# Kernel tuning notes

Measured on AMD Instinct MI355X. Metric: run time of the kernel, lower is better.

## Reference

```python
import jax, jax.numpy as jnp
import numpy as np

T, D, R, C, L = 4096, 512, 32, 32, 2  # time, input, trace, context, num_blocks
NEG_SLOPE = 0.01
EPS = 1e-5  # eqx LayerNorm default


def _layernorm(x, g, b):
    m = jnp.mean(x, -1, keepdims=True)
    v = jnp.var(x, -1, keepdims=True)
    return g * (x - m) * jax.lax.rsqrt(v + EPS) + b


def _ffa_scan(a, b, pre, s0, start):
    # a:[R], b:[C], pre:[T,R,C] real>=0, s0:[1,R,C] complex64, start:[T] bool
    ab = jax.lax.complex(jnp.broadcast_to(-jnp.abs(a)[:, None], (R, C)),
                         jnp.broadcast_to(b[None, :], (R, C)))  # log decay+rotation
    ts = jnp.concatenate([jnp.zeros((1,), jnp.float32), jnp.ones((T,), jnp.float32)])
    vals = jnp.concatenate([s0, pre.astype(jnp.complex64)], axis=0)  # [T+1,R,C]
    rst = jnp.concatenate([jnp.zeros((1,), bool), start])

    def op(l, r):
        tl, sl, dl = l
        tr, sr, dr = r
        decay = jnp.exp(ab[None, :, :] * tr[:, None, None])  # gamma^{t_r}
        s = jnp.where(dr[:, None, None], sr, sr + sl * decay)
        t = jnp.where(dr, tr, tl + tr)
        return (t, s, dl | dr)

    _, states, _ = jax.lax.associative_scan(op, (ts, vals, rst))
    return states[1:]  # [T,R,C]


def _forward(x, start_b, state_real, state_imag, Wt, Wc, a, b,
             W0, b0, g0, beta0, W1, b1, g1, beta1):
    h = x
    z = x
    for i in range(L):
        tr = h @ Wt[i].T  # [T,R]
        ct = h @ Wc[i].T  # [T,R] (source maps context proj to trace_size too; R==C)
        pre = jnp.abs(tr[:, :, None] * ct[:, None, :])  # [T,R,C] outer product
        pre = pre / (1e-8 + jnp.sum(pre, axis=(-2, -1), keepdims=True))
        s0 = jax.lax.complex(state_real[i], state_imag[i])  # [1,R,C]
        states = _ffa_scan(a[i], b[i], pre, s0, start_b)
        s = states.reshape(T, R * C)
        mag = jnp.log1p(jnp.abs(s))
        ang = jnp.angle(s)
        scaled = jnp.concatenate([mag * jnp.sin(ang), mag * jnp.cos(ang)], axis=-1)  # [T,2RC]
        z = jax.nn.leaky_relu(_layernorm(scaled @ W0[i].T + b0[i], g0[i], beta0[i]), NEG_SLOPE)
        z = jax.nn.leaky_relu(_layernorm(z @ W1[i].T + b1[i], g1[i], beta1[i]), NEG_SLOPE)
        h = h + z  # residual feeds next block; NSFFM returns last block's z
    return z


def setup_inputs() -> dict:
    key = jax.random.key(0)
    ks = jax.random.split(key, 8)
    x = jax.random.normal(ks[0], (T, D), jnp.float32)
    start = jax.random.randint(ks[1], (T,), 0, 2).astype(jnp.int32)
    next_done = jax.random.randint(ks[2], (T,), 0, 2).astype(jnp.int32)
    Wt = jax.random.normal(ks[3], (L, R, D), jnp.float32) / np.sqrt(D)
    Wc = jax.random.normal(ks[4], (L, R, D), jnp.float32) / np.sqrt(D)
    # ffa.init: a = linspace decays, b = log-spaced angular frequencies
    a = jnp.broadcast_to(jnp.linspace(1e-6, 0.5, R, dtype=jnp.float32)[None], (L, R)).copy()
    b = jnp.broadcast_to((2 * jnp.pi / jnp.exp(jnp.linspace(np.log(1.0), np.log(1024.0), C))).astype(jnp.float32)[None], (L, C)).copy()
    W0 = jax.random.normal(ks[5], (L, D, 2 * R * C), jnp.float32) * 0.01  # default_init scale=0.01
    W1 = jax.random.normal(ks[6], (L, D, D), jnp.float32) / np.sqrt(D)
    return {
        'x': x, 'start': start, 'next_done': next_done,
        'state_real': jnp.zeros((L, 1, R, C), jnp.float32),
        'state_imag': jnp.zeros((L, 1, R, C), jnp.float32),
        'Wt': Wt, 'Wc': Wc, 'a': a, 'b': b,
        'W0': W0, 'b0': jnp.zeros((L, D), jnp.float32),
        'g0': jnp.ones((L, D), jnp.float32), 'beta0': jnp.zeros((L, D), jnp.float32),
        'W1': W1, 'b1': jnp.zeros((L, D), jnp.float32),
        'g1': jnp.ones((L, D), jnp.float32), 'beta1': jnp.zeros((L, D), jnp.float32),
    }


def reference(x, start, next_done, state_real, state_imag, Wt, Wc, a, b,
              W0, b0, g0, beta0, W1, b1, g1, beta1):
    del next_done  # not used in the scan math (kept for interface parity)
    start_b = start.astype(bool)
    return _forward(x, start_b, state_real, state_imag, Wt, Wc, a, b,
                    W0, b0, g0, beta0, W1, b1, g1, beta1)
```

## Files before the change

kernel.cpp:

```cpp
#include <hip/hip_runtime.h>
#include <math.h>

#define TT 4096
#define DD 512
#define RR 32
#define CC 32
#define RC 1024
#define LL 2
#define CHUNK 32
#define NCHUNK 128
#define NEG_SLOPE 0.01f
#define LN_EPS 1e-5f

typedef __attribute__((ext_vector_type(8))) __bf16 bf16x8;
typedef __attribute__((ext_vector_type(4))) float f32x4;

__device__ __forceinline__ unsigned short f2bf(float f) {
    unsigned int u = __builtin_bit_cast(unsigned int, f);
    u += 0x7fffu + ((u >> 16) & 1u);
    return (unsigned short)(u >> 16);
}

__device__ __forceinline__ void gload16(const unsigned short* g, unsigned short* l) {
    __builtin_amdgcn_global_load_lds(
        (const __attribute__((address_space(1))) unsigned int*)(const void*)g,
        (__attribute__((address_space(3))) unsigned int*)(void*)l,
        16, 0, 0);
}

#define NX4  524288
#define NW04 524288
#define NW14 131072
#define NCV  (NX4 + NW04 + NW14)
#define NPK  16384
__global__ __launch_bounds__(256) void setup_kernel(const float4* __restrict__ x,
                                                    const float4* __restrict__ W0,
                                                    const float4* __restrict__ W1,
                                                    const float* __restrict__ Wt,
                                                    const float* __restrict__ Wc,
                                                    ushort4* __restrict__ xb,
                                                    ushort4* __restrict__ W0b,
                                                    ushort4* __restrict__ W1b,
                                                    ushort4* __restrict__ Wtc) {
    int i = blockIdx.x * 256 + threadIdx.x;
    float4 v;
    ushort4* dst;
    int j;
    if (i < NCV) {
        const float4* src;
        if (i < NX4) { src = x; dst = xb; j = i; }
        else if (i < NX4 + NW04) { src = W0; dst = W0b; j = i - NX4; }
        else { src = W1; dst = W1b; j = i - NX4 - NW04; }
        v = src[j];
    } else {
        int ii = i - NCV;
        if (ii >= NPK) return;
        int e = ii * 4;
        int l = e >> 15;
        int r = (e >> 9) & 63;
        int k = e & 511;
        v = (r < 32) ? *(const float4*)&Wt[((size_t)l * 32 + r) * 512 + k]
                     : *(const float4*)&Wc[((size_t)l * 32 + (r - 32)) * 512 + k];
        dst = Wtc; j = ii;
    }
    ushort4 o;
    o.x = f2bf(v.x); o.y = f2bf(v.y); o.z = f2bf(v.z); o.w = f2bf(v.w);
    dst[j] = o;
}

__global__ __launch_bounds__(256) void proj_denom_kernel(const unsigned short* __restrict__ A,
                                                         const unsigned short* __restrict__ B,
                                                         float* __restrict__ tcabs) {
    __shared__ __align__(16) unsigned short As[64 * 32];
    __shared__ __align__(16) unsigned short Bs[64 * 32];
    const int tid = threadIdx.x;
    const int w = tid >> 6, lane = tid & 63;
    const int bm = blockIdx.x * 64;
    const int K = 512;
    const int srow = tid >> 2;
    const int sl = tid & 3;
    const int sswz = (sl ^ ((srow >> 1) & 3)) * 8;
    const unsigned short* gA = A + (size_t)(bm + srow) * K + sl * 8;
    const unsigned short* gB = B + (size_t)srow * K + sl * 8;
    const int wA = srow * 32 + sswz;
    const int wB = srow * 32 + sswz;
    const int fr = lane & 15, hi = lane >> 4;
    const int kslot = hi ^ ((fr >> 1) & 3);
    f32x4 acc0 = {}, acc1 = {}, acc2 = {}, acc3 = {};

    uint4 va = *(const uint4*)gA;
    uint4 vb = *(const uint4*)gB;
    for (int k0 = 0; k0 < K; k0 += 32) {
        __syncthreads();
        *(uint4*)&As[wA] = va;
        *(uint4*)&Bs[wB] = vb;
        __syncthreads();
        if (k0 + 32 < K) {
            va = *(const uint4*)(gA + k0 + 32);
            vb = *(const uint4*)(gB + k0 + 32);
        }
        const int arow = w * 16 + fr;
        bf16x8 af = *(const bf16x8*)&As[arow * 32 + kslot * 8];
        bf16x8 b0 = *(const bf16x8*)&Bs[(0 * 16 + fr) * 32 + kslot * 8];
        bf16x8 b1 = *(const bf16x8*)&Bs[(1 * 16 + fr) * 32 + kslot * 8];
        bf16x8 b2 = *(const bf16x8*)&Bs[(2 * 16 + fr) * 32 + kslot * 8];
        bf16x8 b3 = *(const bf16x8*)&Bs[(3 * 16 + fr) * 32 + kslot * 8];
        acc0 = __builtin_amdgcn_mfma_f32_16x16x32_bf16(af, b0, acc0, 0, 0, 0);
        acc1 = __builtin_amdgcn_mfma_f32_16x16x32_bf16(af, b1, acc1, 0, 0, 0);
        acc2 = __builtin_amdgcn_mfma_f32_16x16x32_bf16(af, b2, acc2, 0, 0, 0);
        acc3 = __builtin_amdgcn_mfma_f32_16x16x32_bf16(af, b3, acc3, 0, 0, 0);
    }
#pragma unroll
    for (int q = 0; q < 4; ++q) {
        float a0 = fabsf(acc0[q]), a1 = fabsf(acc1[q]);
        float a2 = fabsf(acc2[q]), a3 = fabsf(acc3[q]);
        float st = a0 + a1, sc = a2 + a3;
        st += __shfl_xor(st, 1); sc += __shfl_xor(sc, 1);
        st += __shfl_xor(st, 2); sc += __shfl_xor(sc, 2);
        st += __shfl_xor(st, 4); sc += __shfl_xor(sc, 4);
        st += __shfl_xor(st, 8); sc += __shfl_xor(sc, 8);
        float inv = 1.f / (1e-8f + st * sc);
        size_t rb = (size_t)(bm + w * 16 + hi * 4 + q) * 64;
        tcabs[rb + fr]      = a0 * inv;
        tcabs[rb + fr + 16] = a1 * inv;
        tcabs[rb + fr + 32] = a2;
        tcabs[rb + fr + 48] = a3;
    }
}

__global__ __launch_bounds__(256) void scan_pass1(const float* __restrict__ tcabs,
                                                  const int* __restrict__ start,
                                                  const float* __restrict__ a,
                                                  const float* __restrict__ b,
                                                  float4* __restrict__ ab4) {
    int tid = blockIdx.x * 256 + threadIdx.x;
    int rc = tid & (RC - 1);
    int chunk = tid >> 10;
    int r = rc >> 5, c = rc & 31;
    float e = expf(-fabsf(a[r]));
    float gr = e * cosf(b[c]);
    float gi = e * sinf(b[c]);
    float alr = 1.f, ali = 0.f, ber = 0.f, bei = 0.f;
    int t0 = chunk * CHUNK;
    for (int j = 0; j < CHUNK; ++j) {
        int t = t0 + j;
        float pre = tcabs[t * 64 + r] * tcabs[t * 64 + 32 + c];
        if (start[t]) {
            alr = 0.f; ali = 0.f; ber = pre; bei = 0.f;
        } else {
            float nbr = pre + gr * ber - gi * bei;
            float nbi =       gr * bei + gi * ber;
            float nar = gr * alr - gi * ali;
            float nai = gr * ali + gi * alr;
            ber = nbr; bei = nbi; alr = nar; ali = nai;
        }
    }
    ab4[chunk * RC + rc] = make_float4(alr, ali, ber, bei);
}

__global__ __launch_bounds__(256) void scan_pass2f(const float* __restrict__ tcabs,
                                                   const float4* __restrict__ ab4,
                                                   const int* __restrict__ start,
                                                   const float* __restrict__ a,
                                                   const float* __restrict__ b,
                                                   const float* __restrict__ s0r,
                                                   const float* __restrict__ s0i,
                                                   unsigned short* __restrict__ scaled) {
    int bx = blockIdx.x;
    int chunk = bx >> 2;
    int rc = (bx & 3) * 256 + threadIdx.x;
    int r = rc >> 5, c = rc & 31;
    float e = expf(-fabsf(a[r]));
    float gr = e * cosf(b[c]);
    float gi = e * sinf(b[c]);
    float sr = s0r[rc], si = s0i[rc];
    int j = 0;
    for (; j + 8 <= chunk; j += 8) {
        float4 buf[8];
#pragma unroll
        for (int u = 0; u < 8; ++u) buf[u] = ab4[(j + u) * RC + rc];
#pragma unroll
        for (int u = 0; u < 8; ++u) {
            float nsr = buf[u].z + buf[u].x * sr - buf[u].y * si;
            float nsi = buf[u].w + buf[u].x * si + buf[u].y * sr;
            sr = nsr; si = nsi;
        }
    }
    for (; j < chunk; ++j) {
        float4 ab = ab4[j * RC + rc];
        float nsr = ab.z + ab.x * sr - ab.y * si;
        float nsi = ab.w + ab.x * si + ab.y * sr;
        sr = nsr; si = nsi;
    }
    int t0 = chunk * CHUNK;
    for (int jj = 0; jj < CHUNK; ++jj) {
        int t = t0 + jj;
        float pre = tcabs[t * 64 + r] * tcabs[t * 64 + 32 + c];
        if (start[t]) {
            sr = pre; si = 0.f;
        } else {
            float nsr = pre + gr * sr - gi * si;
            float nsi =       gr * si + gi * sr;
            sr = nsr; si = nsi;
        }
        float m = sqrtf(sr * sr + si * si);
        float mag = log1pf(m);
        float f = (m > 0.f) ? (mag / m) : 0.f;
        scaled[(size_t)t * 2048 + rc]        = f2bf(si * f);
        scaled[(size_t)t * 2048 + 1024 + rc] = f2bf(sr * f);
    }
}

template <int K, int N, int SPLITK>
__global__ __launch_bounds__(256) void gemm_bt_mfma(const unsigned short* __restrict__ A,
                                                    const unsigned short* __restrict__ B,
                                                    float* __restrict__ Cm) {
    __shared__ __align__(16) unsigned short As[128 * 32];
    __shared__ __align__(16) unsigned short Bs[64 * 32];
    const int tid = threadIdx.x;
    const int w = tid >> 6, lane = tid & 63;
    const int nwg = gridDim.x * gridDim.y * gridDim.z;
    const int id = blockIdx.x + gridDim.x * (blockIdx.y + gridDim.y * blockIdx.z);
    const int lid = (id & 7) * (nwg >> 3) + (id >> 3);
    const int bxs = lid % gridDim.x;
    const int t2 = lid / gridDim.x;
    const int bys = t2 % gridDim.y;
    const int bzs = t2 / gridDim.y;
    const int bm = bys * 128, bn = bxs * 64;
    const int kbeg = bzs * (K / SPLITK);
    const int kend = kbeg + (K / SPLITK);
    const int wr = w >> 1, wc = w & 1;
    const int lrow = lane >> 2;
    const int sphys = lane & 3;
    const int slog = sphys ^ ((lrow >> 1) & 3);
    const unsigned short* gA0 = A + (size_t)(bm + w * 32 + lrow) * K + slog * 8;
    const unsigned short* gA1 = A + (size_t)(bm + w * 32 + 16 + lrow) * K + slog * 8;
    const unsigned short* gB  = B + (size_t)(bn + w * 16 + lrow) * K + slog * 8;
    unsigned short* lA0 = &As[(w * 32) * 32];
    unsigned short* lA1 = &As[(w * 32 + 16) * 32];
    unsigned short* lB  = &Bs[(w * 16) * 32];
    const int fr = lane & 15, hi = lane >> 4;
    const int kslot = hi ^ ((fr >> 1) & 3);
    f32x4 acc[4][2] = {};

    for (int k0 = kbeg; k0 < kend; k0 += 32) {
        __syncthreads();
        gload16(gA0 + k0, lA0);
        gload16(gA1 + k0, lA1);
        gload16(gB  + k0, lB);
        __syncthreads();
        bf16x8 af[4], bfv[2];
#pragma unroll
        for (int mi = 0; mi < 4; ++mi) {
            int row = wr * 64 + mi * 16 + fr;
            af[mi] = *(const bf16x8*)&As[row * 32 + kslot * 8];
        }
#pragma unroll
        for (int ni = 0; ni < 2; ++ni) {
            int row = wc * 32 + ni * 16 + fr;
            bfv[ni] = *(const bf16x8*)&Bs[row * 32 + kslot * 8];
        }
#pragma unroll
        for (int mi = 0; mi < 4; ++mi)
#pragma unroll
            for (int ni = 0; ni < 2; ++ni)
                acc[mi][ni] = __builtin_amdgcn_mfma_f32_16x16x32_bf16(
                    af[mi], bfv[ni], acc[mi][ni], 0, 0, 0);
    }
    float* Cz = Cm + (size_t)bzs * TT * N;
    const int ccol0 = bn + wc * 32 + fr;
    const int crow0 = bm + wr * 64 + hi * 4;
#pragma unroll
    for (int ni = 0; ni < 2; ++ni) {
        int col = ccol0 + ni * 16;
#pragma unroll
        for (int mi = 0; mi < 4; ++mi)
#pragma unroll
            for (int q = 0; q < 4; ++q)
                Cz[(size_t)(crow0 + mi * 16 + q) * N + col] = acc[mi][ni][q];
    }
}

__global__ __launch_bounds__(256) void ln_lrelu_kernel(const float* __restrict__ y0,
                                                       const float* __restrict__ y1,
                                                       const float* __restrict__ badd,
                                                       const float* __restrict__ g,
                                                       const float* __restrict__ be,
                                                       unsigned short* __restrict__ zb,
                                                       const float* __restrict__ res,
                                                       unsigned short* __restrict__ hbf,
                                                       float* __restrict__ fout) {
    int t = blockIdx.x;
    int tid = threadIdx.x;
    size_t base = (size_t)t * 512;
    float v0 = y0[base + tid] + y1[base + tid] + badd[tid];
    float v1 = y0[base + 256 + tid] + y1[base + 256 + tid] + badd[256 + tid];
    float s = v0 + v1, ss = v0 * v0 + v1 * v1;
#pragma unroll
    for (int o = 32; o > 0; o >>= 1) {
        s  += __shfl_down(s, o);
        ss += __shfl_down(ss, o);
    }
    __shared__ float sh[8];
    __shared__ float mrs[2];
    int wid = tid >> 6, lane = tid & 63;
    if (lane == 0) { sh[wid] = s; sh[4 + wid] = ss; }
    __syncthreads();
    if (tid == 0) {
        float S = sh[0] + sh[1] + sh[2] + sh[3];
        float SS = sh[4] + sh[5] + sh[6] + sh[7];
        float m = S * (1.f / 512.f);
        float var = SS * (1.f / 512.f) - m * m;
        mrs[0] = m;
        mrs[1] = rsqrtf(var + LN_EPS);
    }
    __syncthreads();
    float m = mrs[0], rs = mrs[1];
    float z0 = g[tid] * (v0 - m) * rs + be[tid];
    float z1 = g[256 + tid] * (v1 - m) * rs + be[256 + tid];
    z0 = (z0 > 0.f) ? z0 : NEG_SLOPE * z0;
    z1 = (z1 > 0.f) ? z1 : NEG_SLOPE * z1;
    if (zb)   { zb[base + tid] = f2bf(z0); zb[base + 256 + tid] = f2bf(z1); }
    if (hbf) {
        float h0 = (res ? res[base + tid] : 0.f) + z0;
        float h1 = (res ? res[base + 256 + tid] : 0.f) + z1;
        hbf[base + tid] = f2bf(h0);
        hbf[base + 256 + tid] = f2bf(h1);
    }
    if (fout) { fout[base + tid] = z0; fout[base + 256 + tid] = z1; }
}

extern "C" void kernel_launch(void* const* d_in, const int* in_sizes, int n_in,
                              void* d_out, int out_size, void* d_ws, size_t ws_size,
                              hipStream_t stream) {
    const float* x     = (const float*)d_in[0];
    const int*   start = (const int*)d_in[1];
    const float* s0r = (const float*)d_in[3];
    const float* s0i = (const float*)d_in[4];
    const float* Wt  = (const float*)d_in[5];
    const float* Wc  = (const float*)d_in[6];
    const float* a   = (const float*)d_in[7];
    const float* b   = (const float*)d_in[8];
    const float* W0  = (const float*)d_in[9];
    const float* b0  = (const float*)d_in[10];
    const float* g0  = (const float*)d_in[11];
    const float* be0 = (const float*)d_in[12];
    const float* W1  = (const float*)d_in[13];
    const float* b1  = (const float*)d_in[14];
    const float* g1  = (const float*)d_in[15];
    const float* be1 = (const float*)d_in[16];
    float* out = (float*)d_out;
    float* ws  = (float*)d_ws;

    float* p = ws;
    float* tcabs  = p; p += 262144;
    float4* ab4   = (float4*)p; p += 524288;
    unsigned short* scaled = (unsigned short*)p; p += 4194304;
    float* ybufp  = p; p += 4194304;
    unsigned short* zbuf_bf = (unsigned short*)p; p += 1048576;
    unsigned short* x_bf    = (unsigned short*)p; p += 1048576;
    unsigned short* h_bf    = (unsigned short*)p; p += 1048576;
    unsigned short* Wtcbf   = (unsigned short*)p; p += 32768;
    unsigned short* W0bf    = (unsigned short*)p; p += 1048576;
    unsigned short* W1bf    = (unsigned short*)p; p += 262144;

    setup_kernel<<<(NCV + NPK + 255) / 256, 256, 0, stream>>>(
        (const float4*)x, (const float4*)W0, (const float4*)W1, Wt, Wc,
        (ushort4*)x_bf, (ushort4*)W0bf, (ushort4*)W1bf, (ushort4*)Wtcbf);

    for (int i = 0; i < LL; ++i) {
        const unsigned short* hb = (i == 0) ? x_bf : h_bf;
        proj_denom_kernel<<<64, 256, 0, stream>>>(
            hb, Wtcbf + (size_t)i * 64 * 512, tcabs);
        scan_pass1<<<NCHUNK * RC / 256, 256, 0, stream>>>(
            tcabs, start, a + i * RR, b + i * CC, ab4);
        scan_pass2f<<<NCHUNK * 4, 256, 0, stream>>>(
            tcabs, ab4, start, a + i * RR, b + i * CC,
            s0r + i * RC, s0i + i * RC, scaled);
        gemm_bt_mfma<2048, 512, 2><<<dim3(8, 32, 2), 256, 0, stream>>>(
            scaled, W0bf + (size_t)i * 512 * 2048, ybufp);
        ln_lrelu_kernel<<<TT, 256, 0, stream>>>(
            ybufp, ybufp + (size_t)TT * 512, b0 + i * DD, g0 + i * DD, be0 + i * DD,
            zbuf_bf, nullptr, nullptr, nullptr);
        gemm_bt_mfma<512, 512, 2><<<dim3(8, 32, 2), 256, 0, stream>>>(
            zbuf_bf, W1bf + (size_t)i * 512 * 512, ybufp);
        ln_lrelu_kernel<<<TT, 256, 0, stream>>>(
            ybufp, ybufp + (size_t)TT * 512, b1 + i * DD, g1 + i * DD, be1 + i * DD,
            nullptr,
            (i < LL - 1) ? x : nullptr,
            (i < LL - 1) ? h_bf : nullptr,
            (i == LL - 1) ? out : nullptr);
    }
}
```

Before: 205.6 us.

## Fuse GEMM with LayerNorm epilogue using full-row tiles and double-buffered loads

```diff
diff --git a/kernel.cpp b/kernel.cpp
--- a/kernel.cpp
+++ b/kernel.cpp
@@ -211,123 +211,99 @@
     }
 }
 
-template <int K, int N, int SPLITK>
-__global__ __launch_bounds__(256) void gemm_bt_mfma(const unsigned short* __restrict__ A,
-                                                    const unsigned short* __restrict__ B,
-                                                    float* __restrict__ Cm) {
-    __shared__ __align__(16) unsigned short As[128 * 32];
-    __shared__ __align__(16) unsigned short Bs[64 * 32];
+template <int K>
+__global__ __launch_bounds__(256) void gemm_ln(const unsigned short* __restrict__ A,
+                                               const unsigned short* __restrict__ B,
+                                               const float* __restrict__ bias,
+                                               const float* __restrict__ g,
+                                               const float* __restrict__ be,
+                                               unsigned short* __restrict__ zb,
+                                               const float* __restrict__ res,
+                                               unsigned short* __restrict__ hbf,
+                                               float* __restrict__ fout) {
+    __shared__ __align__(16) unsigned short As[2][16 * 32];
+    __shared__ __align__(16) unsigned short Bs[2][512 * 32];
+    __shared__ float smem_s[16][4];
+    __shared__ float smem_ss[16][4];
     const int tid = threadIdx.x;
     const int w = tid >> 6, lane = tid & 63;
-    const int nwg = gridDim.x * gridDim.y * gridDim.z;
-    const int id = blockIdx.x + gridDim.x * (blockIdx.y + gridDim.y * blockIdx.z);
-    const int lid = (id & 7) * (nwg >> 3) + (id >> 3);
-    const int bxs = lid % gridDim.x;
-    const int t2 = lid / gridDim.x;
-    const int bys = t2 % gridDim.y;
-    const int bzs = t2 / gridDim.y;
-    const int bm = bys * 128, bn = bxs * 64;
-    const int kbeg = bzs * (K / SPLITK);
-    const int kend = kbeg + (K / SPLITK);
-    const int wr = w >> 1, wc = w & 1;
-    const int lrow = lane >> 2;
-    const int sphys = lane & 3;
-    const int slog = sphys ^ ((lrow >> 1) & 3);
-    const unsigned short* gA0 = A + (size_t)(bm + w * 32 + lrow) * K + slog * 8;
-    const unsigned short* gA1 = A + (size_t)(bm + w * 32 + 16 + lrow) * K + slog * 8;
-    const unsigned short* gB  = B + (size_t)(bn + w * 16 + lrow) * K + slog * 8;
-    unsigned short* lA0 = &As[(w * 32) * 32];
-    unsigned short* lA1 = &As[(w * 32 + 16) * 32];
-    unsigned short* lB  = &Bs[(w * 16) * 32];
+    const int bm = blockIdx.x * 16;
     const int fr = lane & 15, hi = lane >> 4;
     const int kslot = hi ^ ((fr >> 1) & 3);
-    f32x4 acc[4][2] = {};
-
-    for (int k0 = kbeg; k0 < kend; k0 += 32) {
+    const int srow = lane >> 2;
+    const int slog = (lane & 3) ^ ((srow >> 1) & 3);
+    const unsigned short* gBb = B + (size_t)(w * 16 + srow) * K + slog * 8;
+    const unsigned short* gAb = A + (size_t)(bm + srow) * K + slog * 8;
+
+    f32x4 acc[8] = {};
+    constexpr int NT = K / 32;
+
+#pragma unroll
+    for (int u = 0; u < 8; ++u)
+        gload16(gBb + (size_t)u * 64 * K, &Bs[0][(size_t)w * 512 + u * 2048]);
+    if (w == 0) gload16(gAb, &As[0][0]);
+    __syncthreads();
+    int cur = 0;
+    for (int t = 0; t < NT; ++t) {
+        if (t + 1 < NT) {
+            const int k0n = (t + 1) * 32;
+            unsigned short* bd = &Bs[cur ^ 1][(size_t)w * 512];
+#pragma unroll
+            for (int u = 0; u < 8; ++u)
+                gload16(gBb + (size_t)u * 64 * K + k0n, bd + u * 2048);
+            if (w == 0) gload16(gAb + k0n, &As[cur ^ 1][0]);
+        }
+        bf16x8 af = *(const bf16x8*)&As[cur][fr * 32 + kslot * 8];
+#pragma unroll
+        for (int nf = 0; nf < 8; ++nf) {
+            int col = w * 128 + nf * 16 + fr;
+            bf16x8 bv = *(const bf16x8*)&Bs[cur][col * 32 + kslot * 8];
+            acc[nf] = __builtin_amdgcn_mfma_f32_16x16x32_bf16(af, bv, acc[nf], 0, 0, 0);
+        }
         __syncthreads();
-        gload16(gA0 + k0, lA0);
-        gload16(gA1 + k0, lA1);
-        gload16(gB  + k0, lB);
-        __syncthreads();
-        bf16x8 af[4], bfv[2];
-#pragma unroll
-        for (int mi = 0; mi < 4; ++mi) {
-            int row = wr * 64 + mi * 16 + fr;
-            af[mi] = *(const bf16x8*)&As[row * 32 + kslot * 8];
-        }
-#pragma unroll
-        for (int ni = 0; ni < 2; ++ni) {
-            int row = wc * 32 + ni * 16 + fr;
-            bfv[ni] = *(const bf16x8*)&Bs[row * 32 + kslot * 8];
-        }
-#pragma unroll
-        for (int mi = 0; mi < 4; ++mi)
-#pragma unroll
-            for (int ni = 0; ni < 2; ++ni)
-                acc[mi][ni] = __builtin_amdgcn_mfma_f32_16x16x32_bf16(
-                    af[mi], bfv[ni], acc[mi][ni], 0, 0, 0);
-    }
-    float* Cz = Cm + (size_t)bzs * TT * N;
-    const int ccol0 = bn + wc * 32 + fr;
-    const int crow0 = bm + wr * 64 + hi * 4;
-#pragma unroll
-    for (int ni = 0; ni < 2; ++ni) {
-        int col = ccol0 + ni * 16;
-#pragma unroll
-        for (int mi = 0; mi < 4; ++mi)
-#pragma unroll
-            for (int q = 0; q < 4; ++q)
-                Cz[(size_t)(crow0 + mi * 16 + q) * N + col] = acc[mi][ni][q];
-    }
-}
-
-__global__ __launch_bounds__(256) void ln_lrelu_kernel(const float* __restrict__ y0,
-                                                       const float* __restrict__ y1,
-                                                       const float* __restrict__ badd,
-                                                       const float* __restrict__ g,
-                                                       const float* __restrict__ be,
-                                                       unsigned short* __restrict__ zb,
-                                                       const float* __restrict__ res,
-                                                       unsigned short* __restrict__ hbf,
-                                                       float* __restrict__ fout) {
-    int t = blockIdx.x;
-    int tid = threadIdx.x;
-    size_t base = (size_t)t * 512;
-    float v0 = y0[base + tid] + y1[base + tid] + badd[tid];
-    float v1 = y0[base + 256 + tid] + y1[base + 256 + tid] + badd[256 + tid];
-    float s = v0 + v1, ss = v0 * v0 + v1 * v1;
-#pragma unroll
-    for (int o = 32; o > 0; o >>= 1) {
-        s  += __shfl_down(s, o);
-        ss += __shfl_down(ss, o);
-    }
-    __shared__ float sh[8];
-    __shared__ float mrs[2];
-    int wid = tid >> 6, lane = tid & 63;
-    if (lane == 0) { sh[wid] = s; sh[4 + wid] = ss; }
+        cur ^= 1;
+    }
+
+    float bs[8], gs[8], bes[8];
+#pragma unroll
+    for (int nf = 0; nf < 8; ++nf) {
+        int col = w * 128 + nf * 16 + fr;
+        bs[nf] = bias[col]; gs[nf] = g[col]; bes[nf] = be[col];
+    }
+#pragma unroll
+    for (int q = 0; q < 4; ++q) {
+        float s = 0.f, ss = 0.f;
+#pragma unroll
+        for (int nf = 0; nf < 8; ++nf) {
+            float v = acc[nf][q] + bs[nf];
+            s += v; ss += v * v;
+        }
+        s += __shfl_xor(s, 1); ss += __shfl_xor(ss, 1);
+        s += __shfl_xor(s, 2); ss += __shfl_xor(ss, 2);
+        s += __shfl_xor(s, 4); ss += __shfl_xor(ss, 4);
+        s += __shfl_xor(s, 8); ss += __shfl_xor(ss, 8);
+        if (fr == 0) { smem_s[hi * 4 + q][w] = s; smem_ss[hi * 4 + q][w] = ss; }
+    }
     __syncthreads();
-    if (tid == 0) {
-        float S = sh[0] + sh[1] + sh[2] + sh[3];
-        float SS = sh[4] + sh[5] + sh[6] + sh[7];
+#pragma unroll
+    for (int q = 0; q < 4; ++q) {
+        int row = hi * 4 + q;
+        float S  = smem_s[row][0] + smem_s[row][1] + smem_s[row][2] + smem_s[row][3];
+        float SS = smem_ss[row][0] + smem_ss[row][1] + smem_ss[row][2] + smem_ss[row][3];
         float m = S * (1.f / 512.f);
-        float var = SS * (1.f / 512.f) - m * m;
-        mrs[0] = m;
-        mrs[1] = rsqrtf(var + LN_EPS);
-    }
-    __syncthreads();
-    float m = mrs[0], rs = mrs[1];
-    float z0 = g[tid] * (v0 - m) * rs + be[tid];
-    float z1 = g[256 + tid] * (v1 - m) * rs + be[256 + tid];
-    z0 = (z0 > 0.f) ? z0 : NEG_SLOPE * z0;
-    z1 = (z1 > 0.f) ? z1 : NEG_SLOPE * z1;
-    if (zb)   { zb[base + tid] = f2bf(z0); zb[base + 256 + tid] = f2bf(z1); }
-    if (hbf) {
-        float h0 = (res ? res[base + tid] : 0.f) + z0;
-        float h1 = (res ? res[base + 256 + tid] : 0.f) + z1;
-        hbf[base + tid] = f2bf(h0);
-        hbf[base + 256 + tid] = f2bf(h1);
-    }
-    if (fout) { fout[base + tid] = z0; fout[base + 256 + tid] = z1; }
+        float rs = rsqrtf(SS * (1.f / 512.f) - m * m + LN_EPS);
+        size_t rb = (size_t)(bm + row) * 512;
+#pragma unroll
+        for (int nf = 0; nf < 8; ++nf) {
+            int col = w * 128 + nf * 16 + fr;
+            float v = acc[nf][q] + bs[nf];
+            float z = gs[nf] * (v - m) * rs + bes[nf];
+            z = (z > 0.f) ? z : NEG_SLOPE * z;
+            if (zb)   zb[rb + col] = f2bf(z);
+            if (hbf)  hbf[rb + col] = f2bf(res[rb + col] + z);
+            if (fout) fout[rb + col] = z;
+        }
+    }
 }
 
 extern "C" void kernel_launch(void* const* d_in, const int* in_sizes, int n_in,
@@ -356,7 +332,6 @@
     float* tcabs  = p; p += 262144;
     float4* ab4   = (float4*)p; p += 524288;
     unsigned short* scaled = (unsigned short*)p; p += 4194304;
-    float* ybufp  = p; p += 4194304;
     unsigned short* zbuf_bf = (unsigned short*)p; p += 1048576;
     unsigned short* x_bf    = (unsigned short*)p; p += 1048576;
     unsigned short* h_bf    = (unsigned short*)p; p += 1048576;
@@ -377,15 +352,13 @@
         scan_pass2f<<<NCHUNK * 4, 256, 0, stream>>>(
             tcabs, ab4, start, a + i * RR, b + i * CC,
             s0r + i * RC, s0i + i * RC, scaled);
-        gemm_bt_mfma<2048, 512, 2><<<dim3(8, 32, 2), 256, 0, stream>>>(
-            scaled, W0bf + (size_t)i * 512 * 2048, ybufp);
-        ln_lrelu_kernel<<<TT, 256, 0, stream>>>(
-            ybufp, ybufp + (size_t)TT * 512, b0 + i * DD, g0 + i * DD, be0 + i * DD,
+        gemm_ln<2048><<<256, 256, 0, stream>>>(
+            scaled, W0bf + (size_t)i * 512 * 2048,
+            b0 + i * DD, g0 + i * DD, be0 + i * DD,
             zbuf_bf, nullptr, nullptr, nullptr);
-        gemm_bt_mfma<512, 512, 2><<<dim3(8, 32, 2), 256, 0, stream>>>(
-            zbuf_bf, W1bf + (size_t)i * 512 * 512, ybufp);
-        ln_lrelu_kernel<<<TT, 256, 0, stream>>>(
-            ybufp, ybufp + (size_t)TT * 512, b1 + i * DD, g1 + i * DD, be1 + i * DD,
+        gemm_ln<512><<<256, 256, 0, stream>>>(
+            zbuf_bf, W1bf + (size_t)i * 512 * 512,
+            b1 + i * DD, g1 + i * DD, be1 + i * DD,
             nullptr,
             (i < LL - 1) ? x : nullptr,
             (i < LL - 1) ? h_bf : nullptr,
```

Result: slower. 278.0 us (+35.2%).
